# Kernel optimization log

Measured on AMD Instinct MI355X. Metric: run time of the kernel, lower is better.

Reference implementation:

```python
import jax, jax.numpy as jnp
import numpy as np

TOP_K = 2
LOGIT_SCALE = 1.0


def setup_inputs() -> dict:
    key = jax.random.key(0)
    k = jax.random.split(key, 5)
    B, S, C = 1, 1024, 1024
    E, I = 8, 1024           # experts, per-expert intermediate
    x = jax.random.normal(k[0], (B, S, C), dtype=jnp.float32)
    router_w = jax.random.normal(k[1], (E, C), dtype=jnp.float32) * 0.02
    w_in = jax.random.normal(k[2], (E, 2 * I, C), dtype=jnp.float32) * 0.02
    b_in = jnp.zeros((E, 2 * I), dtype=jnp.float32)
    w_out = jax.random.normal(k[3], (E, C, I), dtype=jnp.float32) * 0.02
    b_out = jnp.zeros((E, C), dtype=jnp.float32)
    return {"x": x, "router_w": router_w, "w_in": w_in, "b_in": b_in,
            "w_out": w_out, "b_out": b_out}


def reference(x, router_w, w_in, b_in, w_out, b_out):
    B, S, C = x.shape
    E = router_w.shape[0]
    xt = x.reshape(-1, C)                               # [T, C] flattened tokens
    T = xt.shape[0]

    # Router: softmax over all experts, then top-k probs as combine weights.
    logits = (xt @ router_w.T) * LOGIT_SCALE            # [T, E]
    probs = jax.nn.softmax(logits, axis=-1)
    top_w, top_idx = jax.lax.top_k(probs, TOP_K)        # [T, K]

    # Sparse gate matrix: nonzero only at the top-k experts per token.
    gate = jnp.zeros((T, E), dtype=probs.dtype)
    gate = gate.at[jnp.arange(T)[:, None], top_idx].set(top_w)  # [T, E]

    # Expert SwiGLU MLP, dense over experts, masked combine by gate.
    h = jnp.einsum('tc,eoc->teo', xt, w_in) + b_in      # [T, E, 2I]
    g, u = jnp.split(h, 2, axis=-1)                     # gate / input halves
    a = jax.nn.silu(g) * u                              # swiglu  [T, E, I]
    y = jnp.einsum('tei,eci->tec', a, w_out) + b_out    # [T, E, C]
    out = jnp.einsum('te,tec->tc', gate, y)             # combine top-k experts
    return out.reshape(B, S, C)
```

## Files before the change

kernel.cpp:

```cpp
#include <hip/hip_runtime.h>
#include <hip/hip_bf16.h>
#include <stdint.h>

#define TTOK 1024
#define CDIM 1024
#define NEXP 8
#define IDIM 1024
#define TWOI 2048
#define NSLOT 2048

typedef float f32x4 __attribute__((ext_vector_type(4)));
typedef short s16x8 __attribute__((ext_vector_type(8)));
typedef unsigned short u16;
typedef u16 u16x4 __attribute__((ext_vector_type(4)));
typedef u16 u16x8 __attribute__((ext_vector_type(8)));

__device__ __forceinline__ u16 f2bf(float f) {
  unsigned x = __float_as_uint(f);
  x += 0x7fffu + ((x >> 16) & 1u);
  return (u16)(x >> 16);
}

__device__ __forceinline__ void gload_lds16(const void* g, void* l) {
  __builtin_amdgcn_global_load_lds(
      (const __attribute__((address_space(1))) void*)g,
      (__attribute__((address_space(3))) void*)l, 16, 0, 0);
}

__global__ __launch_bounds__(64) void router_k(const float* __restrict__ x,
                                               const float* __restrict__ rw,
                                               float* __restrict__ topw,
                                               int* __restrict__ topidx,
                                               u16* __restrict__ xb) {
  const int t = blockIdx.x;
  const int lane = threadIdx.x;
  float p[NEXP];
#pragma unroll
  for (int e = 0; e < NEXP; ++e) p[e] = 0.f;
  const float* xr = x + (size_t)t * CDIM;
  u16* xbr = xb + (size_t)t * CDIM;
  for (int c0 = lane * 4; c0 < CDIM; c0 += 64 * 4) {
    f32x4 xv = *(const f32x4*)(xr + c0);
    u16x4 xc;
#pragma unroll
    for (int q = 0; q < 4; ++q) xc[q] = f2bf(xv[q]);
    *(u16x4*)(xbr + c0) = xc;
#pragma unroll
    for (int e = 0; e < NEXP; ++e) {
      f32x4 wv = *(const f32x4*)(rw + (size_t)e * CDIM + c0);
      p[e] += xv[0] * wv[0] + xv[1] * wv[1] + xv[2] * wv[2] + xv[3] * wv[3];
    }
  }
#pragma unroll
  for (int e = 0; e < NEXP; ++e) {
    float v = p[e];
#pragma unroll
    for (int off = 32; off >= 1; off >>= 1) v += __shfl_xor(v, off);
    p[e] = v;
  }
  if (lane == 0) {
    float m = p[0];
#pragma unroll
    for (int e = 1; e < NEXP; ++e) m = fmaxf(m, p[e]);
    float pe[NEXP];
    float den = 0.f;
#pragma unroll
    for (int e = 0; e < NEXP; ++e) { pe[e] = __expf(p[e] - m); den += pe[e]; }
    int i0 = 0;
#pragma unroll
    for (int e = 1; e < NEXP; ++e) if (p[e] > p[i0]) i0 = e;
    int i1 = (i0 == 0) ? 1 : 0;
#pragma unroll
    for (int e = 0; e < NEXP; ++e) if (e != i0 && p[e] > p[i1]) i1 = e;
    const float inv = 1.f / den;
    topw[t * 2] = pe[i0] * inv;
    topw[t * 2 + 1] = pe[i1] * inv;
    topidx[t * 2] = i0;
    topidx[t * 2 + 1] = i1;
  }
}

__global__ __launch_bounds__(1024) void build_k(const int* __restrict__ topidx,
                                                const float* __restrict__ topw,
                                                int* __restrict__ meta,
                                                int* __restrict__ slot_token,
                                                float* __restrict__ gatew) {
  __shared__ int cnt[NEXP], off[NEXP], cur[NEXP];
  const int t = threadIdx.x;
  if (t < NEXP) { cnt[t] = 0; cur[t] = 0; }
  __syncthreads();
  const int e0 = topidx[t * 2];
  const int e1 = topidx[t * 2 + 1];
  atomicAdd(&cnt[e0], 1);
  atomicAdd(&cnt[e1], 1);
  __syncthreads();
  if (t == 0) {
    int acc = 0;
    for (int e = 0; e < NEXP; ++e) { off[e] = acc; acc += cnt[e]; }
  }
  __syncthreads();
  if (t < NEXP) { meta[t] = cnt[t]; meta[16 + t] = off[t]; }
  {
    const int p0 = atomicAdd(&cur[e0], 1);
    const int s0 = off[e0] + p0;
    slot_token[s0] = t;
    gatew[s0] = topw[t * 2];
    const int p1 = atomicAdd(&cur[e1], 1);
    const int s1 = off[e1] + p1;
    slot_token[s1] = t;
    gatew[s1] = topw[t * 2 + 1];
  }
}

__global__ __launch_bounds__(256) void gemm1_k(const u16* __restrict__ A,
                                               const float* __restrict__ W,
                                               const float* __restrict__ b_in,
                                               u16* __restrict__ Aout,
                                               const int* __restrict__ meta,
                                               const int* __restrict__ slot_token) {
  constexpr int BM = 64, K = CDIM;
  const int e = blockIdx.z;
  const int cnt = meta[e];
  const int m0 = blockIdx.y * BM;
  if (m0 >= cnt) return;
  const int off = meta[16 + e];
  const int i0 = blockIdx.x * 32;

  __shared__ u16 sA[2][BM * 64];
  __shared__ u16 sB[2][64 * 64];

  const int tid = threadIdx.x;
  const int lane = tid & 63;
  const int w = tid >> 6;
  const int wr = w >> 1;
  const int wc = w & 1;

  const u16* aSrc[2];
  int aDst[2];
#pragma unroll
  for (int i = 0; i < 2; ++i) {
    const int r = w * 16 + i * 8 + (lane >> 3);
    int rr = m0 + r;
    if (rr > cnt - 1) rr = cnt - 1;
    const int rowg = slot_token[off + rr];
    const int cs = (lane & 7) ^ (r & 7);
    aSrc[i] = A + (size_t)rowg * K + cs * 8;
    aDst[i] = (w * 16 + i * 8) * 64 + lane * 8;
  }

  const int brow = tid >> 2;
  const int bq = tid & 3;
  const int wrow = (brow & 1) ? (IDIM + i0 + (brow >> 1)) : (i0 + (brow >> 1));
  const float* bSrc = W + ((size_t)e * TWOI + wrow) * K + bq * 16;
  const int brow7 = brow & 7;
  const int bOff0 = brow * 64 + (((bq * 2) ^ brow7) * 8);
  const int bOff1 = brow * 64 + (((bq * 2 + 1) ^ brow7) * 8);

  f32x4 acc[2][2];
#pragma unroll
  for (int m = 0; m < 2; ++m)
#pragma unroll
    for (int n = 0; n < 2; ++n) acc[m][n] = (f32x4){0.f, 0.f, 0.f, 0.f};

  {
#pragma unroll
    for (int i = 0; i < 2; ++i) gload_lds16(aSrc[i], &sA[0][aDst[i]]);
    f32x4 v0 = *(const f32x4*)(bSrc);
    f32x4 v1 = *(const f32x4*)(bSrc + 4);
    f32x4 v2 = *(const f32x4*)(bSrc + 8);
    f32x4 v3 = *(const f32x4*)(bSrc + 12);
    u16x8 lo, hi;
#pragma unroll
    for (int q = 0; q < 4; ++q) lo[q] = f2bf(v0[q]);
#pragma unroll
    for (int q = 0; q < 4; ++q) lo[4 + q] = f2bf(v1[q]);
#pragma unroll
    for (int q = 0; q < 4; ++q) hi[q] = f2bf(v2[q]);
#pragma unroll
    for (int q = 0; q < 4; ++q) hi[4 + q] = f2bf(v3[q]);
    *(u16x8*)(&sB[0][bOff0]) = lo;
    *(u16x8*)(&sB[0][bOff1]) = hi;
  }
  __syncthreads();

  int c = 0;
  for (int k0 = 0; k0 < K; k0 += 64) {
    const int nk = k0 + 64;
    const bool has_next = nk < K;
    f32x4 v0, v1, v2, v3;
    if (has_next) {
#pragma unroll
      for (int i = 0; i < 2; ++i) gload_lds16(aSrc[i] + nk, &sA[1 - c][aDst[i]]);
      const float* bs = bSrc + nk;
      v0 = *(const f32x4*)(bs);
      v1 = *(const f32x4*)(bs + 4);
      v2 = *(const f32x4*)(bs + 8);
      v3 = *(const f32x4*)(bs + 12);
    }
#pragma unroll
    for (int kh = 0; kh < 2; ++kh) {
      const int j = kh * 4 + (lane >> 4);
      s16x8 af[2], bf[2];
#pragma unroll
      for (int m = 0; m < 2; ++m) {
        const int r = wr * 32 + m * 16 + (lane & 15);
        af[m] = *(const s16x8*)(&sA[c][r * 64 + ((j ^ (r & 7)) * 8)]);
      }
#pragma unroll
      for (int n = 0; n < 2; ++n) {
        const int r = wc * 32 + n * 16 + (lane & 15);
        bf[n] = *(const s16x8*)(&sB[c][r * 64 + ((j ^ (r & 7)) * 8)]);
      }
#pragma unroll
      for (int m = 0; m < 2; ++m)
#pragma unroll
        for (int n = 0; n < 2; ++n)
          acc[m][n] = __builtin_amdgcn_mfma_f32_16x16x32_bf16(af[m], bf[n], acc[m][n], 0, 0, 0);
    }
    if (has_next) {
      u16x8 lo, hi;
#pragma unroll
      for (int q = 0; q < 4; ++q) lo[q] = f2bf(v0[q]);
#pragma unroll
      for (int q = 0; q < 4; ++q) lo[4 + q] = f2bf(v1[q]);
#pragma unroll
      for (int q = 0; q < 4; ++q) hi[q] = f2bf(v2[q]);
#pragma unroll
      for (int q = 0; q < 4; ++q) hi[4 + q] = f2bf(v3[q]);
      *(u16x8*)(&sB[1 - c][bOff0]) = lo;
      *(u16x8*)(&sB[1 - c][bOff1]) = hi;
    }
    __syncthreads();
    c ^= 1;
  }

#pragma unroll
  for (int m = 0; m < 2; ++m) {
#pragma unroll
    for (int jj = 0; jj < 4; ++jj) {
      const int tr = wr * 32 + m * 16 + ((lane >> 4) * 4) + jj;
      const bool live = (m0 + tr) < cnt;
      const size_t slot = (size_t)(off + m0 + tr);
#pragma unroll
      for (int n = 0; n < 2; ++n) {
        const int cc = wc * 32 + n * 16 + (lane & 15);
        const int wrow_c = (cc & 1) ? (IDIM + i0 + (cc >> 1)) : (i0 + (cc >> 1));
        float v = acc[m][n][jj] + b_in[(size_t)e * TWOI + wrow_c];
        const float vo = __shfl_xor(v, 1);
        if (!(lane & 1) && live) {
          const float g = v, u = vo;
          const float aval = (g / (1.f + __expf(-g))) * u;
          Aout[slot * IDIM + i0 + (cc >> 1)] = f2bf(aval);
        }
      }
    }
  }
}

__global__ __launch_bounds__(256) void gemm2_k(const u16* __restrict__ A,
                                               const float* __restrict__ W,
                                               const float* __restrict__ b_out,
                                               float* __restrict__ out,
                                               const int* __restrict__ meta,
                                               const int* __restrict__ slot_token,
                                               const float* __restrict__ gatew) {
  constexpr int BM = 64, K = IDIM;
  const int e = blockIdx.z;
  const int cnt = meta[e];
  const int m0 = blockIdx.y * BM;
  if (m0 >= cnt) return;
  const int off = meta[16 + e];
  const int n0 = blockIdx.x * 64;

  __shared__ u16 sA[2][BM * 64];
  __shared__ u16 sB[2][64 * 64];

  const int tid = threadIdx.x;
  const int lane = tid & 63;
  const int w = tid >> 6;
  const int wr = w >> 1;
  const int wc = w & 1;

  const u16* aSrc[2];
  int aDst[2];
#pragma unroll
  for (int i = 0; i < 2; ++i) {
    const int r = w * 16 + i * 8 + (lane >> 3);
    int rr = m0 + r;
    if (rr > cnt - 1) rr = cnt - 1;
    const int cs = (lane & 7) ^ (r & 7);
    aSrc[i] = A + (size_t)(off + rr) * K + cs * 8;
    aDst[i] = (w * 16 + i * 8) * 64 + lane * 8;
  }

  const int brow = tid >> 2;
  const int bq = tid & 3;
  const float* bSrc = W + ((size_t)e * CDIM + (n0 + brow)) * K + bq * 16;
  const int brow7 = brow & 7;
  const int bOff0 = brow * 64 + (((bq * 2) ^ brow7) * 8);
  const int bOff1 = brow * 64 + (((bq * 2 + 1) ^ brow7) * 8);

  f32x4 acc[2][2];
#pragma unroll
  for (int m = 0; m < 2; ++m)
#pragma unroll
    for (int n = 0; n < 2; ++n) acc[m][n] = (f32x4){0.f, 0.f, 0.f, 0.f};

  {
#pragma unroll
    for (int i = 0; i < 2; ++i) gload_lds16(aSrc[i], &sA[0][aDst[i]]);
    f32x4 v0 = *(const f32x4*)(bSrc);
    f32x4 v1 = *(const f32x4*)(bSrc + 4);
    f32x4 v2 = *(const f32x4*)(bSrc + 8);
    f32x4 v3 = *(const f32x4*)(bSrc + 12);
    u16x8 lo, hi;
#pragma unroll
    for (int q = 0; q < 4; ++q) lo[q] = f2bf(v0[q]);
#pragma unroll
    for (int q = 0; q < 4; ++q) lo[4 + q] = f2bf(v1[q]);
#pragma unroll
    for (int q = 0; q < 4; ++q) hi[q] = f2bf(v2[q]);
#pragma unroll
    for (int q = 0; q < 4; ++q) hi[4 + q] = f2bf(v3[q]);
    *(u16x8*)(&sB[0][bOff0]) = lo;
    *(u16x8*)(&sB[0][bOff1]) = hi;
  }
  __syncthreads();

  int c = 0;
  for (int k0 = 0; k0 < K; k0 += 64) {
    const int nk = k0 + 64;
    const bool has_next = nk < K;
    f32x4 v0, v1, v2, v3;
    if (has_next) {
#pragma unroll
      for (int i = 0; i < 2; ++i) gload_lds16(aSrc[i] + nk, &sA[1 - c][aDst[i]]);
      const float* bs = bSrc + nk;
      v0 = *(const f32x4*)(bs);
      v1 = *(const f32x4*)(bs + 4);
      v2 = *(const f32x4*)(bs + 8);
      v3 = *(const f32x4*)(bs + 12);
    }
#pragma unroll
    for (int kh = 0; kh < 2; ++kh) {
      const int j = kh * 4 + (lane >> 4);
      s16x8 af[2], bf[2];
#pragma unroll
      for (int m = 0; m < 2; ++m) {
        const int r = wr * 32 + m * 16 + (lane & 15);
        af[m] = *(const s16x8*)(&sA[c][r * 64 + ((j ^ (r & 7)) * 8)]);
      }
#pragma unroll
      for (int n = 0; n < 2; ++n) {
        const int r = wc * 32 + n * 16 + (lane & 15);
        bf[n] = *(const s16x8*)(&sB[c][r * 64 + ((j ^ (r & 7)) * 8)]);
      }
#pragma unroll
      for (int m = 0; m < 2; ++m)
#pragma unroll
        for (int n = 0; n < 2; ++n)
          acc[m][n] = __builtin_amdgcn_mfma_f32_16x16x32_bf16(af[m], bf[n], acc[m][n], 0, 0, 0);
    }
    if (has_next) {
      u16x8 lo, hi;
#pragma unroll
      for (int q = 0; q < 4; ++q) lo[q] = f2bf(v0[q]);
#pragma unroll
      for (int q = 0; q < 4; ++q) lo[4 + q] = f2bf(v1[q]);
#pragma unroll
      for (int q = 0; q < 4; ++q) hi[q] = f2bf(v2[q]);
#pragma unroll
      for (int q = 0; q < 4; ++q) hi[4 + q] = f2bf(v3[q]);
      *(u16x8*)(&sB[1 - c][bOff0]) = lo;
      *(u16x8*)(&sB[1 - c][bOff1]) = hi;
    }
    __syncthreads();
    c ^= 1;
  }

#pragma unroll
  for (int m = 0; m < 2; ++m) {
#pragma unroll
    for (int jj = 0; jj < 4; ++jj) {
      const int tr = wr * 32 + m * 16 + ((lane >> 4) * 4) + jj;
      if (m0 + tr < cnt) {
        const int slot = off + m0 + tr;
        const int tok = slot_token[slot];
        const float gw = gatew[slot];
#pragma unroll
        for (int n = 0; n < 2; ++n) {
          const int col = n0 + wc * 32 + n * 16 + (lane & 15);
          const float v = acc[m][n][jj] + b_out[(size_t)e * CDIM + col];
          atomicAdd(&out[(size_t)tok * CDIM + col], gw * v);
        }
      }
    }
  }
}

extern "C" void kernel_launch(void* const* d_in, const int* in_sizes, int n_in,
                              void* d_out, int out_size, void* d_ws, size_t ws_size,
                              hipStream_t stream) {
  const float* x = (const float*)d_in[0];
  const float* rw = (const float*)d_in[1];
  const float* w_in = (const float*)d_in[2];
  const float* b_in = (const float*)d_in[3];
  const float* w_out = (const float*)d_in[4];
  const float* b_out = (const float*)d_in[5];
  float* out = (float*)d_out;
  char* ws = (char*)d_ws;

  int* meta = (int*)ws;
  int* slot_token = (int*)(ws + 1024);
  float* topw = (float*)(ws + 1024 + 8192);
  int* topidx = (int*)(ws + 1024 + 16384);
  float* gatew = (float*)(ws + 1024 + 24576);
  u16* xb = (u16*)(ws + 65536);
  u16* a = (u16*)(ws + 65536 + (2u << 20));

  hipMemsetAsync(out, 0, (size_t)TTOK * CDIM * sizeof(float), stream);
  router_k<<<TTOK, 64, 0, stream>>>(x, rw, topw, topidx, xb);
  build_k<<<1, 1024, 0, stream>>>(topidx, topw, meta, slot_token, gatew);
  gemm1_k<<<dim3(32, 32, NEXP), 256, 0, stream>>>(
      xb, w_in, b_in, a, meta, slot_token);
  gemm2_k<<<dim3(16, 32, NEXP), 256, 0, stream>>>(
      a, w_out, b_out, out, meta, slot_token, gatew);
}
```

Baseline: 203.1 us.

## Pre-convert expert weights to bf16 and use 3-stage direct-to-LDS pipelines

Adds a kernel that converts w_in and w_out to bf16 in workspace each call, so both GEMMs can load B tiles with global_load_lds instead of loading fp32 into registers and converting. Both GEMMs now use a triple-buffered LDS pipeline with explicit vmcnt waits and barriers. gemm1's M tile doubles to 128, halving grid rows and weight re-reads. The cost is an extra full pass over all weights per call and more LDS use per block.

```diff
diff --git a/kernel.cpp b/kernel.cpp
--- a/kernel.cpp
+++ b/kernel.cpp
@@ -8,6 +8,7 @@
 #define IDIM 1024
 #define TWOI 2048
 #define NSLOT 2048
+#define NSTEP 16
 
 typedef float f32x4 __attribute__((ext_vector_type(4)));
 typedef short s16x8 __attribute__((ext_vector_type(8)));
@@ -15,6 +16,10 @@
 typedef u16 u16x4 __attribute__((ext_vector_type(4)));
 typedef u16 u16x8 __attribute__((ext_vector_type(8)));
 
+#define VMCNT(n) asm volatile("s_waitcnt vmcnt(" #n ")" ::: "memory")
+#define SBAR() __builtin_amdgcn_s_barrier()
+#define SCHED0() __builtin_amdgcn_sched_barrier(0)
+
 __device__ __forceinline__ u16 f2bf(float f) {
   unsigned x = __float_as_uint(f);
   x += 0x7fffu + ((x >> 16) & 1u);
@@ -25,6 +30,30 @@
   __builtin_amdgcn_global_load_lds(
       (const __attribute__((address_space(1))) void*)g,
       (__attribute__((address_space(3))) void*)l, 16, 0, 0);
+}
+
+__global__ __launch_bounds__(256) void cvtw_k(const float* __restrict__ win,
+                                              const float* __restrict__ wout,
+                                              u16* __restrict__ bin,
+                                              u16* __restrict__ bout) {
+  const int NIN = NEXP * TWOI * CDIM;
+  const int NTOT = NIN + NEXP * CDIM * IDIM;
+  for (int i = (blockIdx.x * 256 + threadIdx.x) * 8; i < NTOT;
+       i += gridDim.x * 256 * 8) {
+    const float* src;
+    u16* dst;
+    int j;
+    if (i < NIN) { src = win; dst = bin; j = i; }
+    else         { src = wout; dst = bout; j = i - NIN; }
+    f32x4 v0 = *(const f32x4*)(src + j);
+    f32x4 v1 = *(const f32x4*)(src + j + 4);
+    u16x8 o;
+#pragma unroll
+    for (int q = 0; q < 4; ++q) o[q] = f2bf(v0[q]);
+#pragma unroll
+    for (int q = 0; q < 4; ++q) o[4 + q] = f2bf(v1[q]);
+    *(u16x8*)(dst + j) = o;
+  }
 }
 
 __global__ __launch_bounds__(64) void router_k(const float* __restrict__ x,
@@ -113,12 +142,12 @@
 }
 
 __global__ __launch_bounds__(256) void gemm1_k(const u16* __restrict__ A,
-                                               const float* __restrict__ W,
+                                               const u16* __restrict__ Wb,
                                                const float* __restrict__ b_in,
                                                u16* __restrict__ Aout,
                                                const int* __restrict__ meta,
                                                const int* __restrict__ slot_token) {
-  constexpr int BM = 64, K = CDIM;
+  constexpr int BM = 128, K = CDIM;
   const int e = blockIdx.z;
   const int cnt = meta[e];
   const int m0 = blockIdx.y * BM;
@@ -126,8 +155,8 @@
   const int off = meta[16 + e];
   const int i0 = blockIdx.x * 32;
 
-  __shared__ u16 sA[2][BM * 64];
-  __shared__ u16 sB[2][64 * 64];
+  __shared__ u16 sA[3][BM * 64];
+  __shared__ u16 sB[3][64 * 64];
 
   const int tid = threadIdx.x;
   const int lane = tid & 63;
@@ -135,110 +164,83 @@
   const int wr = w >> 1;
   const int wc = w & 1;
 
-  const u16* aSrc[2];
-  int aDst[2];
-#pragma unroll
-  for (int i = 0; i < 2; ++i) {
-    const int r = w * 16 + i * 8 + (lane >> 3);
+  const u16* aSrc[4];
+  int aDst[4];
+#pragma unroll
+  for (int i = 0; i < 4; ++i) {
+    const int r = w * 32 + i * 8 + (lane >> 3);
     int rr = m0 + r;
     if (rr > cnt - 1) rr = cnt - 1;
     const int rowg = slot_token[off + rr];
     const int cs = (lane & 7) ^ (r & 7);
     aSrc[i] = A + (size_t)rowg * K + cs * 8;
-    aDst[i] = (w * 16 + i * 8) * 64 + lane * 8;
-  }
-
-  const int brow = tid >> 2;
-  const int bq = tid & 3;
-  const int wrow = (brow & 1) ? (IDIM + i0 + (brow >> 1)) : (i0 + (brow >> 1));
-  const float* bSrc = W + ((size_t)e * TWOI + wrow) * K + bq * 16;
-  const int brow7 = brow & 7;
-  const int bOff0 = brow * 64 + (((bq * 2) ^ brow7) * 8);
-  const int bOff1 = brow * 64 + (((bq * 2 + 1) ^ brow7) * 8);
-
-  f32x4 acc[2][2];
-#pragma unroll
-  for (int m = 0; m < 2; ++m)
+    aDst[i] = (w * 32 + i * 8) * 64 + lane * 8;
+  }
+  const u16* bSrc[2];
+  int bDst[2];
+#pragma unroll
+  for (int i = 0; i < 2; ++i) {
+    const int r = w * 16 + i * 8 + (lane >> 3);
+    const int wrow = (r & 1) ? (IDIM + i0 + (r >> 1)) : (i0 + (r >> 1));
+    const int cs = (lane & 7) ^ (r & 7);
+    bSrc[i] = Wb + ((size_t)e * TWOI + wrow) * K + cs * 8;
+    bDst[i] = (w * 16 + i * 8) * 64 + lane * 8;
+  }
+
+  f32x4 acc[4][2];
+#pragma unroll
+  for (int m = 0; m < 4; ++m)
 #pragma unroll
     for (int n = 0; n < 2; ++n) acc[m][n] = (f32x4){0.f, 0.f, 0.f, 0.f};
 
-  {
-#pragma unroll
-    for (int i = 0; i < 2; ++i) gload_lds16(aSrc[i], &sA[0][aDst[i]]);
-    f32x4 v0 = *(const f32x4*)(bSrc);
-    f32x4 v1 = *(const f32x4*)(bSrc + 4);
-    f32x4 v2 = *(const f32x4*)(bSrc + 8);
-    f32x4 v3 = *(const f32x4*)(bSrc + 12);
-    u16x8 lo, hi;
-#pragma unroll
-    for (int q = 0; q < 4; ++q) lo[q] = f2bf(v0[q]);
-#pragma unroll
-    for (int q = 0; q < 4; ++q) lo[4 + q] = f2bf(v1[q]);
-#pragma unroll
-    for (int q = 0; q < 4; ++q) hi[q] = f2bf(v2[q]);
-#pragma unroll
-    for (int q = 0; q < 4; ++q) hi[4 + q] = f2bf(v3[q]);
-    *(u16x8*)(&sB[0][bOff0]) = lo;
-    *(u16x8*)(&sB[0][bOff1]) = hi;
-  }
-  __syncthreads();
-
-  int c = 0;
-  for (int k0 = 0; k0 < K; k0 += 64) {
-    const int nk = k0 + 64;
-    const bool has_next = nk < K;
-    f32x4 v0, v1, v2, v3;
-    if (has_next) {
-#pragma unroll
-      for (int i = 0; i < 2; ++i) gload_lds16(aSrc[i] + nk, &sA[1 - c][aDst[i]]);
-      const float* bs = bSrc + nk;
-      v0 = *(const f32x4*)(bs);
-      v1 = *(const f32x4*)(bs + 4);
-      v2 = *(const f32x4*)(bs + 8);
-      v3 = *(const f32x4*)(bs + 12);
-    }
+  auto STAGE = [&](int t) {
+    const int cb = t % 3;
+    const int ko = t * 64;
+#pragma unroll
+    for (int i = 0; i < 4; ++i) gload_lds16(aSrc[i] + ko, &sA[cb][aDst[i]]);
+#pragma unroll
+    for (int i = 0; i < 2; ++i) gload_lds16(bSrc[i] + ko, &sB[cb][bDst[i]]);
+  };
+  auto COMPUTE = [&](int cb) {
 #pragma unroll
     for (int kh = 0; kh < 2; ++kh) {
       const int j = kh * 4 + (lane >> 4);
-      s16x8 af[2], bf[2];
-#pragma unroll
-      for (int m = 0; m < 2; ++m) {
-        const int r = wr * 32 + m * 16 + (lane & 15);
-        af[m] = *(const s16x8*)(&sA[c][r * 64 + ((j ^ (r & 7)) * 8)]);
+      s16x8 af[4], bf[2];
+#pragma unroll
+      for (int m = 0; m < 4; ++m) {
+        const int r = wr * 64 + m * 16 + (lane & 15);
+        af[m] = *(const s16x8*)(&sA[cb][r * 64 + ((j ^ (r & 7)) * 8)]);
       }
 #pragma unroll
       for (int n = 0; n < 2; ++n) {
         const int r = wc * 32 + n * 16 + (lane & 15);
-        bf[n] = *(const s16x8*)(&sB[c][r * 64 + ((j ^ (r & 7)) * 8)]);
-      }
-#pragma unroll
-      for (int m = 0; m < 2; ++m)
+        bf[n] = *(const s16x8*)(&sB[cb][r * 64 + ((j ^ (r & 7)) * 8)]);
+      }
+#pragma unroll
+      for (int m = 0; m < 4; ++m)
 #pragma unroll
         for (int n = 0; n < 2; ++n)
           acc[m][n] = __builtin_amdgcn_mfma_f32_16x16x32_bf16(af[m], bf[n], acc[m][n], 0, 0, 0);
     }
-    if (has_next) {
-      u16x8 lo, hi;
-#pragma unroll
-      for (int q = 0; q < 4; ++q) lo[q] = f2bf(v0[q]);
-#pragma unroll
-      for (int q = 0; q < 4; ++q) lo[4 + q] = f2bf(v1[q]);
-#pragma unroll
-      for (int q = 0; q < 4; ++q) hi[q] = f2bf(v2[q]);
-#pragma unroll
-      for (int q = 0; q < 4; ++q) hi[4 + q] = f2bf(v3[q]);
-      *(u16x8*)(&sB[1 - c][bOff0]) = lo;
-      *(u16x8*)(&sB[1 - c][bOff1]) = hi;
-    }
-    __syncthreads();
-    c ^= 1;
-  }
-
-#pragma unroll
-  for (int m = 0; m < 2; ++m) {
+  };
+
+  STAGE(0);
+  STAGE(1);
+  for (int t = 0; t < NSTEP - 2; ++t) {
+    STAGE(t + 2);
+    VMCNT(12); SCHED0();
+    SBAR();
+    COMPUTE(t % 3);
+    SBAR();
+  }
+  VMCNT(6); SCHED0(); SBAR(); COMPUTE((NSTEP - 2) % 3); SBAR();
+  VMCNT(0); SCHED0(); SBAR(); COMPUTE((NSTEP - 1) % 3);
+
+#pragma unroll
+  for (int m = 0; m < 4; ++m) {
 #pragma unroll
     for (int jj = 0; jj < 4; ++jj) {
-      const int tr = wr * 32 + m * 16 + ((lane >> 4) * 4) + jj;
+      const int tr = wr * 64 + m * 16 + ((lane >> 4) * 4) + jj;
       const bool live = (m0 + tr) < cnt;
       const size_t slot = (size_t)(off + m0 + tr);
 #pragma unroll
@@ -258,7 +260,7 @@
 }
 
 __global__ __launch_bounds__(256) void gemm2_k(const u16* __restrict__ A,
-                                               const float* __restrict__ W,
+                                               const u16* __restrict__ Wb,
                                                const float* __restrict__ b_out,
                                                float* __restrict__ out,
                                                const int* __restrict__ meta,
@@ -272,8 +274,8 @@
   const int off = meta[16 + e];
   const int n0 = blockIdx.x * 64;
 
-  __shared__ u16 sA[2][BM * 64];
-  __shared__ u16 sB[2][64 * 64];
+  __shared__ u16 sA[3][BM * 64];
+  __shared__ u16 sB[3][64 * 64];
 
   const int tid = threadIdx.x;
   const int lane = tid & 63;
@@ -292,13 +294,15 @@
     aSrc[i] = A + (size_t)(off + rr) * K + cs * 8;
     aDst[i] = (w * 16 + i * 8) * 64 + lane * 8;
   }
-
-  const int brow = tid >> 2;
-  const int bq = tid & 3;
-  const float* bSrc = W + ((size_t)e * CDIM + (n0 + brow)) * K + bq * 16;
-  const int brow7 = brow & 7;
-  const int bOff0 = brow * 64 + (((bq * 2) ^ brow7) * 8);
-  const int bOff1 = brow * 64 + (((bq * 2 + 1) ^ brow7) * 8);
+  const u16* bSrc[2];
+  int bDst[2];
+#pragma unroll
+  for (int i = 0; i < 2; ++i) {
+    const int r = w * 16 + i * 8 + (lane >> 3);
+    const int cs = (lane & 7) ^ (r & 7);
+    bSrc[i] = Wb + ((size_t)e * CDIM + (n0 + r)) * K + cs * 8;
+    bDst[i] = (w * 16 + i * 8) * 64 + lane * 8;
+  }
 
   f32x4 acc[2][2];
 #pragma unroll
@@ -306,41 +310,15 @@
 #pragma unroll
     for (int n = 0; n < 2; ++n) acc[m][n] = (f32x4){0.f, 0.f, 0.f, 0.f};
 
-  {
-#pragma unroll
-    for (int i = 0; i < 2; ++i) gload_lds16(aSrc[i], &sA[0][aDst[i]]);
-    f32x4 v0 = *(const f32x4*)(bSrc);
-    f32x4 v1 = *(const f32x4*)(bSrc + 4);
-    f32x4 v2 = *(const f32x4*)(bSrc + 8);
-    f32x4 v3 = *(const f32x4*)(bSrc + 12);
-    u16x8 lo, hi;
-#pragma unroll
-    for (int q = 0; q < 4; ++q) lo[q] = f2bf(v0[q]);
-#pragma unroll
-    for (int q = 0; q < 4; ++q) lo[4 + q] = f2bf(v1[q]);
-#pragma unroll
-    for (int q = 0; q < 4; ++q) hi[q] = f2bf(v2[q]);
-#pragma unroll
-    for (int q = 0; q < 4; ++q) hi[4 + q] = f2bf(v3[q]);
-    *(u16x8*)(&sB[0][bOff0]) = lo;
-    *(u16x8*)(&sB[0][bOff1]) = hi;
-  }
-  __syncthreads();
-
-  int c = 0;
-  for (int k0 = 0; k0 < K; k0 += 64) {
-    const int nk = k0 + 64;
-    const bool has_next = nk < K;
-    f32x4 v0, v1, v2, v3;
-    if (has_next) {
-#pragma unroll
-      for (int i = 0; i < 2; ++i) gload_lds16(aSrc[i] + nk, &sA[1 - c][aDst[i]]);
-      const float* bs = bSrc + nk;
-      v0 = *(const f32x4*)(bs);
-      v1 = *(const f32x4*)(bs + 4);
-      v2 = *(const f32x4*)(bs + 8);
-      v3 = *(const f32x4*)(bs + 12);
-    }
+  auto STAGE = [&](int t) {
+    const int cb = t % 3;
+    const int ko = t * 64;
+#pragma unroll
+    for (int i = 0; i < 2; ++i) gload_lds16(aSrc[i] + ko, &sA[cb][aDst[i]]);
+#pragma unroll
+    for (int i = 0; i < 2; ++i) gload_lds16(bSrc[i] + ko, &sB[cb][bDst[i]]);
+  };
+  auto COMPUTE = [&](int cb) {
 #pragma unroll
     for (int kh = 0; kh < 2; ++kh) {
       const int j = kh * 4 + (lane >> 4);
@@ -348,12 +326,12 @@
 #pragma unroll
       for (int m = 0; m < 2; ++m) {
         const int r = wr * 32 + m * 16 + (lane & 15);
-        af[m] = *(const s16x8*)(&sA[c][r * 64 + ((j ^ (r & 7)) * 8)]);
+        af[m] = *(const s16x8*)(&sA[cb][r * 64 + ((j ^ (r & 7)) * 8)]);
       }
 #pragma unroll
       for (int n = 0; n < 2; ++n) {
         const int r = wc * 32 + n * 16 + (lane & 15);
-        bf[n] = *(const s16x8*)(&sB[c][r * 64 + ((j ^ (r & 7)) * 8)]);
+        bf[n] = *(const s16x8*)(&sB[cb][r * 64 + ((j ^ (r & 7)) * 8)]);
       }
 #pragma unroll
       for (int m = 0; m < 2; ++m)
@@ -361,22 +339,19 @@
         for (int n = 0; n < 2; ++n)
           acc[m][n] = __builtin_amdgcn_mfma_f32_16x16x32_bf16(af[m], bf[n], acc[m][n], 0, 0, 0);
     }
-    if (has_next) {
-      u16x8 lo, hi;
-#pragma unroll
-      for (int q = 0; q < 4; ++q) lo[q] = f2bf(v0[q]);
-#pragma unroll
-      for (int q = 0; q < 4; ++q) lo[4 + q] = f2bf(v1[q]);
-#pragma unroll
-      for (int q = 0; q < 4; ++q) hi[q] = f2bf(v2[q]);
-#pragma unroll
-      for (int q = 0; q < 4; ++q) hi[4 + q] = f2bf(v3[q]);
-      *(u16x8*)(&sB[1 - c][bOff0]) = lo;
-      *(u16x8*)(&sB[1 - c][bOff1]) = hi;
-    }
-    __syncthreads();
-    c ^= 1;
-  }
+  };
+
+  STAGE(0);
+  STAGE(1);
+  for (int t = 0; t < NSTEP - 2; ++t) {
+    STAGE(t + 2);
+    VMCNT(8); SCHED0();
+    SBAR();
+    COMPUTE(t % 3);
+    SBAR();
+  }
+  VMCNT(4); SCHED0(); SBAR(); COMPUTE((NSTEP - 2) % 3); SBAR();
+  VMCNT(0); SCHED0(); SBAR(); COMPUTE((NSTEP - 1) % 3);
 
 #pragma unroll
   for (int m = 0; m < 2; ++m) {
@@ -417,12 +392,15 @@
   float* gatew = (float*)(ws + 1024 + 24576);
   u16* xb = (u16*)(ws + 65536);
   u16* a = (u16*)(ws + 65536 + (2u << 20));
+  u16* wbin = (u16*)(ws + 65536 + (6u << 20));
+  u16* wbout = (u16*)(ws + 65536 + (38u << 20));
 
   hipMemsetAsync(out, 0, (size_t)TTOK * CDIM * sizeof(float), stream);
+  cvtw_k<<<2048, 256, 0, stream>>>(w_in, w_out, wbin, wbout);
   router_k<<<TTOK, 64, 0, stream>>>(x, rw, topw, topidx, xb);
   build_k<<<1, 1024, 0, stream>>>(topidx, topw, meta, slot_token, gatew);
-  gemm1_k<<<dim3(32, 32, NEXP), 256, 0, stream>>>(
-      xb, w_in, b_in, a, meta, slot_token);
+  gemm1_k<<<dim3(32, 16, NEXP), 256, 0, stream>>>(
+      xb, wbin, b_in, a, meta, slot_token);
   gemm2_k<<<dim3(16, 32, NEXP), 256, 0, stream>>>(
-      a, w_out, b_out, out, meta, slot_token, gatew);
-}
+      a, wbout, b_out, out, meta, slot_token, gatew);
+}
```

New measurement: 192.8 us. 1.05x faster.
